# Performance work log

Hardware: AMD Instinct MI355X
Metric: run time of the kernel (lower is better)

Reference implementation:

```python
import jax, jax.numpy as jnp
import numpy as np

DIM = 576
NUM_HEADS = 1
HEAD_DIM = DIM // NUM_HEADS
SCALE = HEAD_DIM ** -0.5


def layer_norm(x, w, b, eps=1e-5):
    mu = jnp.mean(x, axis=-1, keepdims=True)
    var = jnp.var(x, axis=-1, keepdims=True)
    return (x - mu) * jax.lax.rsqrt(var + eps) * w + b


def setup_inputs() -> dict:
    key = jax.random.key(0)
    ks = jax.random.split(key, 10)
    B, N, C = 8, 2048, DIM
    s = C ** -0.5
    return {
        "x": jax.random.normal(ks[0], (B, N, C), jnp.float32),
        "y": jax.random.normal(ks[1], (B, N, C), jnp.float32),
        "Wq": jax.random.normal(ks[2], (C, C), jnp.float32) * s,
        "Wk": jax.random.normal(ks[3], (C, C), jnp.float32) * s,
        "Wv": jax.random.normal(ks[4], (C, C), jnp.float32) * s,
        "Wp": jax.random.normal(ks[5], (C, C), jnp.float32) * s,
        "bp": jnp.zeros((C,), jnp.float32),
        "gx": jnp.ones((C,), jnp.float32), "bx": jnp.zeros((C,), jnp.float32),
        "gy": jnp.ones((C,), jnp.float32), "by": jnp.zeros((C,), jnp.float32),
        "gz": jnp.ones((C,), jnp.float32), "bz": jnp.zeros((C,), jnp.float32),
    }


def reference(x, y, Wq, Wk, Wv, Wp, bp, gx, bx, gy, by, gz, bz):
    B, N, C = x.shape
    H, D = NUM_HEADS, HEAD_DIM
    xn = layer_norm(x, gx, bx)
    yn = layer_norm(y, gy, by)
    # torch Linear: out = in @ W^T
    q = (yn @ Wq.T).reshape(B, N, H, D).transpose(0, 2, 1, 3)  # [B,H,N,D]
    k = (xn @ Wk.T).reshape(B, N, H, D).transpose(0, 2, 1, 3)
    v = (xn @ Wv.T).reshape(B, N, H, D).transpose(0, 2, 1, 3)
    attn = jax.nn.sigmoid(jnp.einsum("bhnd,bhmd->bhnm", q, k) * SCALE)
    out = jnp.einsum("bhnm,bhmd->bhnd", attn, v).transpose(0, 2, 1, 3).reshape(B, N, C)
    out = out @ Wp.T + bp
    out = out + xn  # residual with normalized x
    return layer_norm(out, gz, bz)
```

## Files before the change

kernel.cpp:

```cpp
#include <hip/hip_runtime.h>

typedef __bf16 bfrag __attribute__((ext_vector_type(8)));
typedef float f32x4 __attribute__((ext_vector_type(4)));

__device__ __forceinline__ unsigned short f2bf(float f) {
    unsigned int u = __float_as_uint(f);
    unsigned int r = (u + 0x7fffu + ((u >> 16) & 1u)) >> 16;
    return (unsigned short)r;
}
__device__ __forceinline__ float bf2f(unsigned short h) {
    return __uint_as_float(((unsigned int)h) << 16);
}

__device__ __forceinline__ void gll16(const unsigned short* g, unsigned short* l) {
    __builtin_amdgcn_global_load_lds(
        (const __attribute__((address_space(1))) unsigned int*)g,
        (__attribute__((address_space(3))) unsigned int*)l, 16, 0, 0);
}

template<int BM, int BN, int WR, int WC, int EPI>
__global__ __launch_bounds__(256) void gemm_nt(
    const unsigned short* __restrict__ A, const unsigned short* __restrict__ B,
    unsigned short* __restrict__ Cb, float* __restrict__ Cf,
    const unsigned short* __restrict__ R, const float* __restrict__ bias,
    int M, int N, int K, float scale,
    size_t sAz, size_t sBz, size_t sCz)
{
    constexpr int BK = 32;
    constexpr int WTM = BM / (WR * 16);
    constexpr int WTN = BN / (WC * 16);
    __shared__ unsigned short sA[BM * BK];
    __shared__ unsigned short sB[BN * BK];

    A += blockIdx.z * sAz;
    B += blockIdx.z * sBz;

    const int tid  = threadIdx.x;
    const int wave = tid >> 6;
    const int lane = tid & 63;
    const int wm = wave / WC;
    const int wn = wave % WC;
    const int bm0 = blockIdx.x * BM;
    const int bn0 = blockIdx.y * BN;
    const int mrow = lane & 15;
    const int kgrp = lane >> 4;

    f32x4 acc[WTM][WTN] = {};

    for (int k0 = 0; k0 < K; k0 += BK) {
        #pragma unroll
        for (int i = 0; i < BM / 64; ++i) {
            int idx = tid + i * 256;
            int r = idx >> 2, c = idx & 3;
            gll16(A + (size_t)(bm0 + r) * K + k0 + c * 8, &sA[idx * 8]);
        }
        #pragma unroll
        for (int i = 0; i < BN / 64; ++i) {
            int idx = tid + i * 256;
            int r = idx >> 2, c = idx & 3;
            gll16(B + (size_t)(bn0 + r) * K + k0 + c * 8, &sB[idx * 8]);
        }
        __syncthreads();

        bfrag af[WTM], bfr[WTN];
        #pragma unroll
        for (int mt = 0; mt < WTM; ++mt)
            af[mt] = *(const bfrag*)&sA[(wm * WTM * 16 + mt * 16 + mrow) * BK + kgrp * 8];
        #pragma unroll
        for (int nt = 0; nt < WTN; ++nt)
            bfr[nt] = *(const bfrag*)&sB[(wn * WTN * 16 + nt * 16 + mrow) * BK + kgrp * 8];
        #pragma unroll
        for (int mt = 0; mt < WTM; ++mt)
            #pragma unroll
            for (int nt = 0; nt < WTN; ++nt)
                acc[mt][nt] = __builtin_amdgcn_mfma_f32_16x16x32_bf16(af[mt], bfr[nt], acc[mt][nt], 0, 0, 0);
        __syncthreads();
    }

    #pragma unroll
    for (int mt = 0; mt < WTM; ++mt) {
        #pragma unroll
        for (int nt = 0; nt < WTN; ++nt) {
            int grow0 = bm0 + wm * WTM * 16 + mt * 16 + kgrp * 4;
            int gcol  = bn0 + wn * WTN * 16 + nt * 16 + mrow;
            #pragma unroll
            for (int r = 0; r < 4; ++r) {
                float v = acc[mt][nt][r];
                size_t off = blockIdx.z * sCz + (size_t)(grow0 + r) * N + gcol;
                if (EPI == 0) {
                    Cb[off] = f2bf(v * scale);
                } else if (EPI == 1) {
                    Cb[off] = f2bf(1.0f / (1.0f + __expf(-v)));
                } else {
                    Cf[off] = v + bias[gcol] + bf2f(R[off]);
                }
            }
        }
    }
}

__global__ __launch_bounds__(256) void qkv_proj(
    const unsigned short* __restrict__ xn, const unsigned short* __restrict__ yn,
    const unsigned short* __restrict__ W,
    unsigned short* __restrict__ qk,
    unsigned short* __restrict__ vt,
    float scale)
{
    constexpr int BM = 128, BN = 64, BK = 32;
    __shared__ unsigned short sA[BM * BK];
    __shared__ unsigned short sB[BN * BK];

    const int z = blockIdx.z;
    const unsigned short* A = (z == 0) ? yn : xn;
    const unsigned short* B = W + (size_t)z * 576 * 576;
    const float sc = (z == 0) ? scale : 1.0f;

    const int tid  = threadIdx.x;
    const int wave = tid >> 6;
    const int lane = tid & 63;
    const int wm = wave >> 1;
    const int wn = wave & 1;
    const int bm0 = blockIdx.x * BM;
    const int bn0 = blockIdx.y * BN;
    const int mrow = lane & 15;
    const int kgrp = lane >> 4;
    constexpr int WTM = 4, WTN = 2;

    f32x4 acc[WTM][WTN] = {};

    for (int k0 = 0; k0 < 576; k0 += BK) {
        #pragma unroll
        for (int i = 0; i < BM / 64; ++i) {
            int idx = tid + i * 256;
            int r = idx >> 2, c = idx & 3;
            gll16(A + (size_t)(bm0 + r) * 576 + k0 + c * 8, &sA[idx * 8]);
        }
        {
            int r = tid >> 2, c = tid & 3;
            gll16(B + (size_t)(bn0 + r) * 576 + k0 + c * 8, &sB[tid * 8]);
        }
        __syncthreads();

        bfrag af[WTM], bfr[WTN];
        #pragma unroll
        for (int mt = 0; mt < WTM; ++mt)
            af[mt] = *(const bfrag*)&sA[(wm * WTM * 16 + mt * 16 + mrow) * BK + kgrp * 8];
        #pragma unroll
        for (int nt = 0; nt < WTN; ++nt)
            bfr[nt] = *(const bfrag*)&sB[(wn * WTN * 16 + nt * 16 + mrow) * BK + kgrp * 8];
        #pragma unroll
        for (int mt = 0; mt < WTM; ++mt)
            #pragma unroll
            for (int nt = 0; nt < WTN; ++nt)
                acc[mt][nt] = __builtin_amdgcn_mfma_f32_16x16x32_bf16(af[mt], bfr[nt], acc[mt][nt], 0, 0, 0);
        __syncthreads();
    }

    #pragma unroll
    for (int mt = 0; mt < WTM; ++mt) {
        #pragma unroll
        for (int nt = 0; nt < WTN; ++nt) {
            int grow0 = bm0 + wm * WTM * 16 + mt * 16 + kgrp * 4;
            int gcol  = bn0 + wn * WTN * 16 + nt * 16 + mrow;
            if (z == 2) {
                ushort4 o;
                o.x = f2bf(acc[mt][nt][0]);
                o.y = f2bf(acc[mt][nt][1]);
                o.z = f2bf(acc[mt][nt][2]);
                o.w = f2bf(acc[mt][nt][3]);
                size_t dst = (((size_t)(grow0 >> 11) * 576 + gcol) << 11) + (grow0 & 2047);
                *(ushort4*)(vt + dst) = o;
            } else {
                unsigned short* C = qk + (size_t)z * 16384 * 576;
                #pragma unroll
                for (int r = 0; r < 4; ++r)
                    C[(size_t)(grow0 + r) * 576 + gcol] = f2bf(acc[mt][nt][r] * sc);
            }
        }
    }
}

__global__ __launch_bounds__(256) void ln_pair(
    const float* __restrict__ x, const float* __restrict__ gx, const float* __restrict__ bx,
    unsigned short* __restrict__ xn,
    const float* __restrict__ y, const float* __restrict__ gy, const float* __restrict__ by,
    unsigned short* __restrict__ yn)
{
    const float* src = blockIdx.y ? y : x;
    const float* g   = blockIdx.y ? gy : gx;
    const float* bb  = blockIdx.y ? by : bx;
    unsigned short* o = blockIdx.y ? yn : xn;

    const int row  = blockIdx.x * 4 + (threadIdx.x >> 6);
    const int lane = threadIdx.x & 63;
    const float* xr = src + (size_t)row * 576;
    float vals[9];
    float s = 0.f, ss = 0.f;
    #pragma unroll
    for (int i = 0; i < 9; ++i) {
        float v = xr[lane + i * 64];
        vals[i] = v; s += v; ss += v * v;
    }
    #pragma unroll
    for (int off = 32; off > 0; off >>= 1) {
        s  += __shfl_xor(s, off, 64);
        ss += __shfl_xor(ss, off, 64);
    }
    float mean = s * (1.0f / 576.0f);
    float var  = ss * (1.0f / 576.0f) - mean * mean;
    float rstd = rsqrtf(var + 1e-5f);
    #pragma unroll
    for (int i = 0; i < 9; ++i) {
        int c = lane + i * 64;
        o[(size_t)row * 576 + c] = f2bf((vals[i] - mean) * rstd * g[c] + bb[c]);
    }
}

__global__ __launch_bounds__(256) void ln_final(
    const float* __restrict__ x, const float* __restrict__ g,
    const float* __restrict__ bb, float* __restrict__ outp)
{
    const int row  = blockIdx.x * 4 + (threadIdx.x >> 6);
    const int lane = threadIdx.x & 63;
    const float* xr = x + (size_t)row * 576;
    float vals[9];
    float s = 0.f, ss = 0.f;
    #pragma unroll
    for (int i = 0; i < 9; ++i) {
        float v = xr[lane + i * 64];
        vals[i] = v; s += v; ss += v * v;
    }
    #pragma unroll
    for (int off = 32; off > 0; off >>= 1) {
        s  += __shfl_xor(s, off, 64);
        ss += __shfl_xor(ss, off, 64);
    }
    float mean = s * (1.0f / 576.0f);
    float var  = ss * (1.0f / 576.0f) - mean * mean;
    float rstd = rsqrtf(var + 1e-5f);
    #pragma unroll
    for (int i = 0; i < 9; ++i) {
        int c = lane + i * 64;
        outp[(size_t)row * 576 + c] = (vals[i] - mean) * rstd * g[c] + bb[c];
    }
}

__global__ __launch_bounds__(256) void cvt4w(
    const float* __restrict__ s0, const float* __restrict__ s1,
    const float* __restrict__ s2, const float* __restrict__ s3,
    unsigned short* __restrict__ dst)
{
    const float* srcs[4] = {s0, s1, s2, s3};
    const float* src = srcs[blockIdx.y];
    unsigned short* d = dst + (size_t)blockIdx.y * 576 * 576;
    int i = (blockIdx.x * 256 + threadIdx.x) * 4;
    float4 f = *(const float4*)(src + i);
    ushort4 o;
    o.x = f2bf(f.x); o.y = f2bf(f.y); o.z = f2bf(f.z); o.w = f2bf(f.w);
    *(ushort4*)(d + i) = o;
}

extern "C" void kernel_launch(void* const* d_in, const int* in_sizes, int n_in,
                              void* d_out, int out_size, void* d_ws, size_t ws_size,
                              hipStream_t stream)
{
    const float* x  = (const float*)d_in[0];
    const float* y  = (const float*)d_in[1];
    const float* Wq = (const float*)d_in[2];
    const float* Wk = (const float*)d_in[3];
    const float* Wv = (const float*)d_in[4];
    const float* Wp = (const float*)d_in[5];
    const float* bp = (const float*)d_in[6];
    const float* gx = (const float*)d_in[7];
    const float* bx = (const float*)d_in[8];
    const float* gy = (const float*)d_in[9];
    const float* by = (const float*)d_in[10];
    const float* gz = (const float*)d_in[11];
    const float* bz = (const float*)d_in[12];

    constexpr size_t WB = 576 * 576 * 2;
    constexpr size_t XB = 16384ull * 576 * 2;
    constexpr size_t TOK = (size_t)2048 * 576;
    constexpr size_t SB  = (size_t)2048 * 2048;

    char* w = (char*)d_ws;
    unsigned short* wq = (unsigned short*)(w);
    unsigned short* wp = (unsigned short*)(w + 3 * WB);
    unsigned short* xn = (unsigned short*)(w + 4 * WB);
    unsigned short* yn = (unsigned short*)(w + 4 * WB + XB);
    unsigned short* q  = (unsigned short*)(w + 4 * WB + 2 * XB);
    unsigned short* k  = (unsigned short*)(w + 4 * WB + 3 * XB);
    unsigned short* vt = (unsigned short*)(w + 4 * WB + 4 * XB);
    unsigned short* S  = (unsigned short*)(w + 4 * WB + 5 * XB);
    unsigned short* attno = yn;
    float* T = (float*)q;

    cvt4w<<<dim3(324, 4), 256, 0, stream>>>(Wq, Wk, Wv, Wp, wq);

    ln_pair<<<dim3(4096, 2), 256, 0, stream>>>(x, gx, bx, xn, y, gy, by, yn);

    const float SCALE = 0.041666666666666664f;
    qkv_proj<<<dim3(128, 9, 3), 256, 0, stream>>>(xn, yn, wq, q, vt, SCALE);

    gemm_nt<128, 128, 2, 2, 1><<<dim3(16, 16, 8), 256, 0, stream>>>(
        q, k, S, nullptr, nullptr, nullptr, 2048, 2048, 576, 1.0f, TOK, TOK, SB);
    gemm_nt<128, 64, 2, 2, 0><<<dim3(16, 9, 8), 256, 0, stream>>>(
        S, vt, attno, nullptr, nullptr, nullptr, 2048, 576, 2048, 1.0f, SB, TOK, TOK);

    gemm_nt<128, 64, 2, 2, 2><<<dim3(128, 9, 1), 256, 0, stream>>>(
        attno, wp, nullptr, T, xn, bp, 16384, 576, 576, 1.0f, 0, 0, 0);
    ln_final<<<4096, 256, 0, stream>>>(T, gz, bz, (float*)d_out);
}
```

Before: 371.5 us.

## Double GEMM K-tile with XOR-swizzled LDS, reorder grid, bf16 projection output

Raises the K tile from 32 to 64 in all GEMMs, which halves the number of barrier-synchronised iterations. Shared-memory tiles now use an XOR-swizzled layout so that MFMA fragment reads avoid bank conflicts. The grid axes are swapped so consecutive blocks share the same A row-tile, which should improve L2 reuse. The output-projection result is now stored as bf16 instead of fp32, cutting traffic into the final layernorm at some cost in precision.

```diff
diff --git a/kernel.cpp b/kernel.cpp
--- a/kernel.cpp
+++ b/kernel.cpp
@@ -18,15 +18,19 @@
         (__attribute__((address_space(3))) unsigned int*)l, 16, 0, 0);
 }
 
+__device__ __forceinline__ int swz(int r, int kc) {
+    return (r >> 3) * 512 + (((r & 7) * 8 + (kc ^ (r & 7))) * 8);
+}
+
 template<int BM, int BN, int WR, int WC, int EPI>
 __global__ __launch_bounds__(256) void gemm_nt(
     const unsigned short* __restrict__ A, const unsigned short* __restrict__ B,
-    unsigned short* __restrict__ Cb, float* __restrict__ Cf,
+    unsigned short* __restrict__ Cb,
     const unsigned short* __restrict__ R, const float* __restrict__ bias,
     int M, int N, int K, float scale,
     size_t sAz, size_t sBz, size_t sCz)
 {
-    constexpr int BK = 32;
+    constexpr int BK = 64;
     constexpr int WTM = BM / (WR * 16);
     constexpr int WTN = BN / (WC * 16);
     __shared__ unsigned short sA[BM * BK];
@@ -36,12 +40,14 @@
     B += blockIdx.z * sBz;
 
     const int tid  = threadIdx.x;
-    const int wave = tid >> 6;
+    const int w    = tid >> 6;
     const int lane = tid & 63;
-    const int wm = wave / WC;
-    const int wn = wave % WC;
-    const int bm0 = blockIdx.x * BM;
-    const int bn0 = blockIdx.y * BN;
+    const int wm = w / WC;
+    const int wn = w % WC;
+    const int bn0 = blockIdx.x * BN;
+    const int bm0 = blockIdx.y * BM;
+    const int rl  = lane >> 3;
+    const int kcs = (lane & 7) ^ rl;
     const int mrow = lane & 15;
     const int kgrp = lane >> 4;
 
@@ -49,31 +55,34 @@
 
     for (int k0 = 0; k0 < K; k0 += BK) {
         #pragma unroll
-        for (int i = 0; i < BM / 64; ++i) {
-            int idx = tid + i * 256;
-            int r = idx >> 2, c = idx & 3;
-            gll16(A + (size_t)(bm0 + r) * K + k0 + c * 8, &sA[idx * 8]);
-        }
-        #pragma unroll
-        for (int i = 0; i < BN / 64; ++i) {
-            int idx = tid + i * 256;
-            int r = idx >> 2, c = idx & 3;
-            gll16(B + (size_t)(bn0 + r) * K + k0 + c * 8, &sB[idx * 8]);
+        for (int i = 0; i < BM / 32; ++i) {
+            int wc = w * (BM / 32) + i;
+            gll16(A + (size_t)(bm0 + wc * 8 + rl) * K + k0 + kcs * 8,
+                  &sA[wc * 512 + lane * 8]);
+        }
+        #pragma unroll
+        for (int i = 0; i < BN / 32; ++i) {
+            int wc = w * (BN / 32) + i;
+            gll16(B + (size_t)(bn0 + wc * 8 + rl) * K + k0 + kcs * 8,
+                  &sB[wc * 512 + lane * 8]);
         }
         __syncthreads();
 
-        bfrag af[WTM], bfr[WTN];
-        #pragma unroll
-        for (int mt = 0; mt < WTM; ++mt)
-            af[mt] = *(const bfrag*)&sA[(wm * WTM * 16 + mt * 16 + mrow) * BK + kgrp * 8];
-        #pragma unroll
-        for (int nt = 0; nt < WTN; ++nt)
-            bfr[nt] = *(const bfrag*)&sB[(wn * WTN * 16 + nt * 16 + mrow) * BK + kgrp * 8];
-        #pragma unroll
-        for (int mt = 0; mt < WTM; ++mt)
+        #pragma unroll
+        for (int kh = 0; kh < 2; ++kh) {
+            bfrag af[WTM], bfr[WTN];
+            #pragma unroll
+            for (int mt = 0; mt < WTM; ++mt)
+                af[mt] = *(const bfrag*)&sA[swz(wm * WTM * 16 + mt * 16 + mrow, kh * 4 + kgrp)];
             #pragma unroll
             for (int nt = 0; nt < WTN; ++nt)
-                acc[mt][nt] = __builtin_amdgcn_mfma_f32_16x16x32_bf16(af[mt], bfr[nt], acc[mt][nt], 0, 0, 0);
+                bfr[nt] = *(const bfrag*)&sB[swz(wn * WTN * 16 + nt * 16 + mrow, kh * 4 + kgrp)];
+            #pragma unroll
+            for (int mt = 0; mt < WTM; ++mt)
+                #pragma unroll
+                for (int nt = 0; nt < WTN; ++nt)
+                    acc[mt][nt] = __builtin_amdgcn_mfma_f32_16x16x32_bf16(af[mt], bfr[nt], acc[mt][nt], 0, 0, 0);
+        }
         __syncthreads();
     }
 
@@ -92,7 +101,7 @@
                 } else if (EPI == 1) {
                     Cb[off] = f2bf(1.0f / (1.0f + __expf(-v)));
                 } else {
-                    Cf[off] = v + bias[gcol] + bf2f(R[off]);
+                    Cb[off] = f2bf(v + bias[gcol] + bf2f(R[off]));
                 }
             }
         }
@@ -106,7 +115,8 @@
     unsigned short* __restrict__ vt,
     float scale)
 {
-    constexpr int BM = 128, BN = 64, BK = 32;
+    constexpr int BM = 128, BN = 64, BK = 64;
+    constexpr int WTM = 4, WTN = 2;
     __shared__ unsigned short sA[BM * BK];
     __shared__ unsigned short sB[BN * BK];
 
@@ -116,43 +126,49 @@
     const float sc = (z == 0) ? scale : 1.0f;
 
     const int tid  = threadIdx.x;
-    const int wave = tid >> 6;
+    const int w    = tid >> 6;
     const int lane = tid & 63;
-    const int wm = wave >> 1;
-    const int wn = wave & 1;
-    const int bm0 = blockIdx.x * BM;
-    const int bn0 = blockIdx.y * BN;
+    const int wm = w >> 1;
+    const int wn = w & 1;
+    const int bn0 = blockIdx.x * BN;
+    const int bm0 = blockIdx.y * BM;
+    const int rl  = lane >> 3;
+    const int kcs = (lane & 7) ^ rl;
     const int mrow = lane & 15;
     const int kgrp = lane >> 4;
-    constexpr int WTM = 4, WTN = 2;
 
     f32x4 acc[WTM][WTN] = {};
 
     for (int k0 = 0; k0 < 576; k0 += BK) {
         #pragma unroll
-        for (int i = 0; i < BM / 64; ++i) {
-            int idx = tid + i * 256;
-            int r = idx >> 2, c = idx & 3;
-            gll16(A + (size_t)(bm0 + r) * 576 + k0 + c * 8, &sA[idx * 8]);
-        }
-        {
-            int r = tid >> 2, c = tid & 3;
-            gll16(B + (size_t)(bn0 + r) * 576 + k0 + c * 8, &sB[tid * 8]);
+        for (int i = 0; i < BM / 32; ++i) {
+            int wc = w * (BM / 32) + i;
+            gll16(A + (size_t)(bm0 + wc * 8 + rl) * 576 + k0 + kcs * 8,
+                  &sA[wc * 512 + lane * 8]);
+        }
+        #pragma unroll
+        for (int i = 0; i < BN / 32; ++i) {
+            int wc = w * (BN / 32) + i;
+            gll16(B + (size_t)(bn0 + wc * 8 + rl) * 576 + k0 + kcs * 8,
+                  &sB[wc * 512 + lane * 8]);
         }
         __syncthreads();
 
-        bfrag af[WTM], bfr[WTN];
-        #pragma unroll
-        for (int mt = 0; mt < WTM; ++mt)
-            af[mt] = *(const bfrag*)&sA[(wm * WTM * 16 + mt * 16 + mrow) * BK + kgrp * 8];
-        #pragma unroll
-        for (int nt = 0; nt < WTN; ++nt)
-            bfr[nt] = *(const bfrag*)&sB[(wn * WTN * 16 + nt * 16 + mrow) * BK + kgrp * 8];
-        #pragma unroll
-        for (int mt = 0; mt < WTM; ++mt)
+        #pragma unroll
+        for (int kh = 0; kh < 2; ++kh) {
+            bfrag af[WTM], bfr[WTN];
+            #pragma unroll
+            for (int mt = 0; mt < WTM; ++mt)
+                af[mt] = *(const bfrag*)&sA[swz(wm * WTM * 16 + mt * 16 + mrow, kh * 4 + kgrp)];
             #pragma unroll
             for (int nt = 0; nt < WTN; ++nt)
-                acc[mt][nt] = __builtin_amdgcn_mfma_f32_16x16x32_bf16(af[mt], bfr[nt], acc[mt][nt], 0, 0, 0);
+                bfr[nt] = *(const bfrag*)&sB[swz(wn * WTN * 16 + nt * 16 + mrow, kh * 4 + kgrp)];
+            #pragma unroll
+            for (int mt = 0; mt < WTM; ++mt)
+                #pragma unroll
+                for (int nt = 0; nt < WTN; ++nt)
+                    acc[mt][nt] = __builtin_amdgcn_mfma_f32_16x16x32_bf16(af[mt], bfr[nt], acc[mt][nt], 0, 0, 0);
+        }
         __syncthreads();
     }
 
@@ -217,17 +233,17 @@
 }
 
 __global__ __launch_bounds__(256) void ln_final(
-    const float* __restrict__ x, const float* __restrict__ g,
+    const unsigned short* __restrict__ x, const float* __restrict__ g,
     const float* __restrict__ bb, float* __restrict__ outp)
 {
     const int row  = blockIdx.x * 4 + (threadIdx.x >> 6);
     const int lane = threadIdx.x & 63;
-    const float* xr = x + (size_t)row * 576;
+    const unsigned short* xr = x + (size_t)row * 576;
     float vals[9];
     float s = 0.f, ss = 0.f;
     #pragma unroll
     for (int i = 0; i < 9; ++i) {
-        float v = xr[lane + i * 64];
+        float v = bf2f(xr[lane + i * 64]);
         vals[i] = v; s += v; ss += v * v;
     }
     #pragma unroll
@@ -293,21 +309,21 @@
     unsigned short* vt = (unsigned short*)(w + 4 * WB + 4 * XB);
     unsigned short* S  = (unsigned short*)(w + 4 * WB + 5 * XB);
     unsigned short* attno = yn;
-    float* T = (float*)q;
+    unsigned short* T = q;
 
     cvt4w<<<dim3(324, 4), 256, 0, stream>>>(Wq, Wk, Wv, Wp, wq);
 
     ln_pair<<<dim3(4096, 2), 256, 0, stream>>>(x, gx, bx, xn, y, gy, by, yn);
 
     const float SCALE = 0.041666666666666664f;
-    qkv_proj<<<dim3(128, 9, 3), 256, 0, stream>>>(xn, yn, wq, q, vt, SCALE);
+    qkv_proj<<<dim3(9, 128, 3), 256, 0, stream>>>(xn, yn, wq, q, vt, SCALE);
 
     gemm_nt<128, 128, 2, 2, 1><<<dim3(16, 16, 8), 256, 0, stream>>>(
-        q, k, S, nullptr, nullptr, nullptr, 2048, 2048, 576, 1.0f, TOK, TOK, SB);
-    gemm_nt<128, 64, 2, 2, 0><<<dim3(16, 9, 8), 256, 0, stream>>>(
-        S, vt, attno, nullptr, nullptr, nullptr, 2048, 576, 2048, 1.0f, SB, TOK, TOK);
-
-    gemm_nt<128, 64, 2, 2, 2><<<dim3(128, 9, 1), 256, 0, stream>>>(
-        attno, wp, nullptr, T, xn, bp, 16384, 576, 576, 1.0f, 0, 0, 0);
+        q, k, S, nullptr, nullptr, 2048, 2048, 576, 1.0f, TOK, TOK, SB);
+    gemm_nt<128, 64, 2, 2, 0><<<dim3(9, 16, 8), 256, 0, stream>>>(
+        S, vt, attno, nullptr, nullptr, 2048, 576, 2048, 1.0f, SB, TOK, TOK);
+
+    gemm_nt<128, 64, 2, 2, 2><<<dim3(9, 128, 1), 256, 0, stream>>>(
+        attno, wp, T, xn, bp, 16384, 576, 576, 1.0f, 0, 0, 0);
     ln_final<<<4096, 256, 0, stream>>>(T, gz, bz, (float*)d_out);
 }
```

After: 424.0 us. +14.1%, slower.
